# Performance work log

Hardware: AMD Instinct MI355X
Metric: run time of the kernel (lower is better)

Reference implementation:

```python
import jax, jax.numpy as jnp
import numpy as np

DIM = 1024
HEADS = 16
HEAD_DIM = DIM // HEADS
SCALE = HEAD_DIM ** -0.5


def setup_inputs() -> dict:
    key = jax.random.key(0)
    k1, k2, k3, k4 = jax.random.split(key, 4)
    x = jax.random.normal(k1, (8, 1024, DIM), dtype=jnp.float32)
    # qkv: Linear(dim, 3*dim), bias=False; proj: Linear(dim, dim) with bias
    w_qkv = jax.random.normal(k2, (DIM, 3 * DIM), dtype=jnp.float32) * (DIM ** -0.5)
    w_proj = jax.random.normal(k3, (DIM, DIM), dtype=jnp.float32) * (DIM ** -0.5)
    b_proj = jax.random.normal(k4, (DIM,), dtype=jnp.float32) * 0.02
    return {"x": x, "w_qkv": w_qkv, "w_proj": w_proj, "b_proj": b_proj}


def reference(x, w_qkv, w_proj, b_proj):
    b, n, dim = x.shape
    h, d = HEADS, HEAD_DIM
    qkv = x @ w_qkv                                  # [b, n, 3*dim]
    qkv = qkv.reshape(b, n, 3, h, d)                  # split (qkv h d)
    q = jnp.transpose(qkv[:, :, 0], (0, 2, 1, 3))     # [b, h, n, d]
    k = jnp.transpose(qkv[:, :, 1], (0, 2, 1, 3))
    v = jnp.transpose(qkv[:, :, 2], (0, 2, 1, 3))
    dots = jnp.einsum('bhid,bhjd->bhij', q, k) * SCALE
    attn = jax.nn.softmax(dots, axis=-1)              # [b, h, n, n]
    out = jnp.einsum('bhij,bhjd->bhid', attn, v)      # [b, h, n, d]
    out = jnp.transpose(out, (0, 2, 1, 3)).reshape(b, n, dim)
    return out @ w_proj + b_proj
```

## Files before the change

### kernel.cpp

```cpp
#include <hip/hip_runtime.h>
#include <hip/hip_bf16.h>
#include <stdint.h>


typedef __attribute__((ext_vector_type(8))) short  short8;
typedef __attribute__((ext_vector_type(4))) float  floatx4;

#define MFMA_BF16(a, b, c) __builtin_amdgcn_mfma_f32_16x16x32_bf16((a), (b), (c), 0, 0, 0)

__device__ __forceinline__ uint16_t f2b(float f) {
    uint32_t i; __builtin_memcpy(&i, &f, 4);
    uint32_t r = i + 0x7FFFu + ((i >> 16) & 1u);
    return (uint16_t)(r >> 16);
}

#if defined(__has_builtin)
#if __has_builtin(__builtin_amdgcn_cvt_pk_bf16_f32)
#define HAVE_PK_BF16 1
#endif
#endif

__device__ __forceinline__ uint32_t pk_bf16(float a, float b) {
#ifdef HAVE_PK_BF16
    typedef __attribute__((ext_vector_type(2))) __bf16 bf16x2;
    bf16x2 v = __builtin_amdgcn_cvt_pk_bf16_f32(a, b);
    uint32_t u; __builtin_memcpy(&u, &v, 4); return u;
#else
    return (uint32_t)f2b(a) | ((uint32_t)f2b(b) << 16);
#endif
}

__device__ __forceinline__ void async16(uint16_t* lds, const uint16_t* g) {
    __builtin_amdgcn_global_load_lds(
        (const __attribute__((address_space(1))) uint32_t*)g,
        (__attribute__((address_space(3))) uint32_t*)lds,
        16, 0, 0);
}

__global__ __launch_bounds__(256) void cvt_f32_bf16(
    const float* __restrict__ in, uint16_t* __restrict__ out, int n4)
{
    const int i = blockIdx.x * 256 + threadIdx.x;
    if (i < n4) {
        const float4 v = ((const float4*)in)[i];
        ushort4 o;
        o.x = f2b(v.x); o.y = f2b(v.y); o.z = f2b(v.z); o.w = f2b(v.w);
        ((ushort4*)out)[i] = o;
    }
}

__global__ __launch_bounds__(256) void transpose_k(
    const float* __restrict__ in, uint16_t* __restrict__ out, int R, int C)
{
    __shared__ uint16_t t[32][33];
    const int bx = blockIdx.x * 32;
    const int by = blockIdx.y * 32;
    const int tx = threadIdx.x & 31, ty = threadIdx.x >> 5;
    #pragma unroll
    for (int j = 0; j < 32; j += 8)
        t[ty + j][tx] = f2b(in[(size_t)(by + ty + j) * C + bx + tx]);
    __syncthreads();
    #pragma unroll
    for (int j = 0; j < 32; j += 8)
        out[(size_t)(bx + ty + j) * R + by + tx] = t[tx][ty + j];
}

template <int EPI>
__global__ __launch_bounds__(256, 2) void gemm_bt(
    const uint16_t* __restrict__ A, const uint16_t* __restrict__ Bt,
    uint16_t* __restrict__ C, float* __restrict__ Cf,
    const float* __restrict__ bias, int M, int N, int K)
{
    __shared__ uint16_t As[128 * 64];
    __shared__ uint16_t Bs[128 * 64];

    const int tid  = threadIdx.x;
    const int lane = tid & 63, quad = lane >> 4, l16 = lane & 15;
    const int wv   = tid >> 6;
    const int wm   = (wv >> 1) * 64, wn = (wv & 1) * 64;

    const int lid = blockIdx.y * gridDim.x + blockIdx.x;
    const int nxl = gridDim.x >> 3;
    const int xcd = lid & 7, loc = lid >> 3;
    const int bx  = xcd * nxl + (loc % nxl);
    const int by  = loc / nxl;
    const int tm  = by * 128, tn = bx * 128;

    floatx4 acc[4][4] = {};

    for (int kt = 0; kt < K; kt += 64) {
        __syncthreads();
        #pragma unroll
        for (int i = 0; i < 4; i++) {
            const int li  = i * 256 + tid;
            const int row = li >> 3;
            const int cg  = (li & 7) ^ (row & 7);
            async16(&As[li * 8], &A[(size_t)(tm + row) * K + kt + cg * 8]);
        }
        #pragma unroll
        for (int i = 0; i < 4; i++) {
            const int li  = i * 256 + tid;
            const int row = li >> 3;
            const int cg  = (li & 7) ^ (row & 7);
            async16(&Bs[li * 8], &Bt[(size_t)(tn + row) * K + kt + cg * 8]);
        }
        __syncthreads();
        #pragma unroll
        for (int kc = 0; kc < 2; kc++) {
            short8 af[4], bf[4];
            #pragma unroll
            for (int mb = 0; mb < 4; mb++) {
                const int row = wm + mb * 16 + l16;
                const int g   = kc * 4 + quad;
                af[mb] = *(const short8*)&As[row * 64 + ((g ^ (row & 7)) * 8)];
            }
            #pragma unroll
            for (int nb = 0; nb < 4; nb++) {
                const int row = wn + nb * 16 + l16;
                const int g   = kc * 4 + quad;
                bf[nb] = *(const short8*)&Bs[row * 64 + ((g ^ (row & 7)) * 8)];
            }
            #pragma unroll
            for (int mb = 0; mb < 4; mb++)
                #pragma unroll
                for (int nb = 0; nb < 4; nb++)
                    acc[mb][nb] = MFMA_BF16(af[mb], bf[nb], acc[mb][nb]);
        }
    }

    if (EPI == 0) {
        const int which = (tn + wn) >> 10;
        if (which == 2) {
            #pragma unroll
            for (int nb = 0; nb < 4; nb++) {
                const int col = tn + wn + nb * 16 + l16;
                const int hh = (col >> 6) & 15, dd = col & 63;
                #pragma unroll
                for (int mb = 0; mb < 4; mb++) {
                    const int gm = tm + wm + mb * 16 + quad * 4;
                    const int b  = gm >> 10, n = gm & 1023;
                    const size_t rgn = (size_t)(256 + b * 16 + hh) * 65536;
                    uint2 o;
                    o.x = pk_bf16(acc[mb][nb][0], acc[mb][nb][1]);
                    o.y = pk_bf16(acc[mb][nb][2], acc[mb][nb][3]);
                    *(uint2*)&C[rgn + (size_t)dd * 1024 + n] = o;
                }
            }
        } else {
            const float qs = (which == 0) ? 0.18033688011112043f : 1.0f;
            #pragma unroll
            for (int nb = 0; nb < 4; nb++) {
                const int col = tn + wn + nb * 16 + l16;
                const int hh = (col >> 6) & 15, dd = col & 63;
                #pragma unroll
                for (int mb = 0; mb < 4; mb++)
                    #pragma unroll
                    for (int r = 0; r < 4; r++) {
                        const int gm = tm + wm + mb * 16 + quad * 4 + r;
                        const int b  = gm >> 10, n = gm & 1023;
                        const size_t rgn = (size_t)(which * 128 + b * 16 + hh) * 65536;
                        C[rgn + (size_t)n * 64 + dd] = f2b(acc[mb][nb][r] * qs);
                    }
            }
        }
    } else {
        #pragma unroll
        for (int nb = 0; nb < 4; nb++) {
            const int col = tn + wn + nb * 16 + l16;
            const float bv = bias[col];
            #pragma unroll
            for (int mb = 0; mb < 4; mb++)
                #pragma unroll
                for (int r = 0; r < 4; r++) {
                    const int gm = tm + wm + mb * 16 + quad * 4 + r;
                    Cf[(size_t)gm * N + col] = acc[mb][nb][r] + bv;
                }
        }
    }
}

__global__ __launch_bounds__(256, 3) void attn_fa(
    const uint16_t* __restrict__ qkv, uint16_t* __restrict__ out)
{
    __shared__ uint16_t Ks[128 * 64];
    __shared__ uint16_t Vs[64 * 128];
    __shared__ uint16_t Ps[4][32 * 72];

    const int tid  = threadIdx.x;
    const int lane = tid & 63, quad = lane >> 4, l16 = lane & 15;
    const int wv   = tid >> 6;
    const int bh   = blockIdx.y;
    const int q0   = blockIdx.x * 128 + wv * 32;

    const size_t qbase  = (size_t)bh * 65536;
    const size_t kbase  = (size_t)(128 + bh) * 65536;
    const size_t vtbase = (size_t)(256 + bh) * 65536;

    short8 qf[2][2];
    #pragma unroll
    for (int nq = 0; nq < 2; nq++)
        #pragma unroll
        for (int ks = 0; ks < 2; ks++)
            qf[nq][ks] = *(const short8*)&qkv[qbase + (size_t)(q0 + nq * 16 + l16) * 64 + ks * 32 + quad * 8];

    floatx4 Oacc[2][4] = {};
    float lpart[2] = {0.f, 0.f};

    for (int kb = 0; kb < 8; kb++) {
        __syncthreads();
        #pragma unroll
        for (int i = 0; i < 4; i++) {
            const int li  = i * 256 + tid;
            const int row = li >> 3;
            const int cg  = (li & 7) ^ (row & 7);
            async16(&Ks[li * 8], &qkv[kbase + (size_t)(kb * 128 + row) * 64 + cg * 8]);
        }
        #pragma unroll
        for (int i = 0; i < 4; i++) {
            const int li  = i * 256 + tid;
            const int row = li >> 4;
            const int cg  = (li & 15) ^ (row & 15);
            async16(&Vs[li * 8], &qkv[vtbase + (size_t)row * 1024 + kb * 128 + cg * 8]);
        }
        __syncthreads();

        #pragma unroll
        for (int h = 0; h < 2; h++) {
            floatx4 st[4][2];
            #pragma unroll
            for (int mb = 0; mb < 4; mb++) {
                const int krow = h * 64 + mb * 16 + l16;
                const int g0 = quad, g1 = 4 + quad;
                short8 kf0 = *(const short8*)&Ks[krow * 64 + ((g0 ^ (krow & 7)) * 8)];
                short8 kf1 = *(const short8*)&Ks[krow * 64 + ((g1 ^ (krow & 7)) * 8)];
                #pragma unroll
                for (int nq = 0; nq < 2; nq++) {
                    floatx4 z = {};
                    z = MFMA_BF16(kf0, qf[nq][0], z);
                    z = MFMA_BF16(kf1, qf[nq][1], z);
                    st[mb][nq] = z;
                }
            }
            #pragma unroll
            for (int mb = 0; mb < 4; mb++)
                #pragma unroll
                for (int nq = 0; nq < 2; nq++)
                    #pragma unroll
                    for (int r = 0; r < 4; r++) {
                        const float p = exp2f(st[mb][nq][r]);
                        st[mb][nq][r] = p;
                        lpart[nq] += p;
                    }
            #pragma unroll
            for (int nq = 0; nq < 2; nq++)
                #pragma unroll
                for (int mb = 0; mb < 4; mb++) {
                    uint2 w;
                    w.x = pk_bf16(st[mb][nq][0], st[mb][nq][1]);
                    w.y = pk_bf16(st[mb][nq][2], st[mb][nq][3]);
                    *(uint2*)&Ps[wv][(nq * 16 + l16) * 72 + mb * 16 + quad * 4] = w;
                }
            short8 pf[2][2];
            #pragma unroll
            for (int qb = 0; qb < 2; qb++)
                #pragma unroll
                for (int kk = 0; kk < 2; kk++)
                    pf[qb][kk] = *(const short8*)&Ps[wv][(qb * 16 + l16) * 72 + kk * 32 + quad * 8];
            #pragma unroll
            for (int nb = 0; nb < 4; nb++)
                #pragma unroll
                for (int kk = 0; kk < 2; kk++) {
                    const int vrow = nb * 16 + l16;
                    const int g    = h * 8 + kk * 4 + quad;
                    short8 vf = *(const short8*)&Vs[vrow * 128 + ((g ^ (vrow & 15)) * 8)];
                    #pragma unroll
                    for (int qb = 0; qb < 2; qb++)
                        Oacc[qb][nb] = MFMA_BF16(pf[qb][kk], vf, Oacc[qb][nb]);
                }
        }
    }

    float linv[2];
    #pragma unroll
    for (int nq = 0; nq < 2; nq++) {
        float l = lpart[nq];
        l += __shfl_xor(l, 16);
        l += __shfl_xor(l, 32);
        linv[nq] = 1.f / l;
    }
    float inv[2][4];
    #pragma unroll
    for (int qb = 0; qb < 2; qb++)
        #pragma unroll
        for (int r = 0; r < 4; r++)
            inv[qb][r] = __shfl(linv[qb], quad * 4 + r);

    const int b = bh >> 4, hh = bh & 15;
    #pragma unroll
    for (int qb = 0; qb < 2; qb++)
        #pragma unroll
        for (int nb = 0; nb < 4; nb++)
            #pragma unroll
            for (int r = 0; r < 4; r++) {
                const int n = q0 + qb * 16 + quad * 4 + r;
                out[((size_t)(b * 1024 + n)) * 1024 + hh * 64 + nb * 16 + l16] =
                    f2b(Oacc[qb][nb][r] * inv[qb][r]);
            }
}

extern "C" void kernel_launch(void* const* d_in, const int* in_sizes, int n_in,
                              void* d_out, int out_size, void* d_ws, size_t ws_size,
                              hipStream_t stream)
{
    const float* x      = (const float*)d_in[0];
    const float* w_qkv  = (const float*)d_in[1];
    const float* w_proj = (const float*)d_in[2];
    const float* b_proj = (const float*)d_in[3];
    float* out = (float*)d_out;

    uint16_t* ws   = (uint16_t*)d_ws;
    uint16_t* xb   = ws;
    uint16_t* wTq  = xb  + 8192 * 1024;
    uint16_t* wTp  = wTq + 3072 * 1024;
    uint16_t* qkvb = wTp + 1024 * 1024;
    uint16_t* ao   = xb;

    cvt_f32_bf16<<<8192, 256, 0, stream>>>(x, xb, 8192 * 1024 / 4);
    transpose_k<<<dim3(96, 32), 256, 0, stream>>>(w_qkv, wTq, 1024, 3072);
    transpose_k<<<dim3(32, 32), 256, 0, stream>>>(w_proj, wTp, 1024, 1024);
    gemm_bt<0><<<dim3(24, 64), 256, 0, stream>>>(xb, wTq, qkvb, nullptr, nullptr, 8192, 3072, 1024);
    attn_fa<<<dim3(8, 128), 256, 0, stream>>>(qkvb, ao);
    gemm_bt<1><<<dim3(8, 64), 256, 0, stream>>>(ao, wTp, nullptr, out, b_proj, 8192, 1024, 1024);
}
```

Before: 242.9 us.

## Redistribute softmax probabilities via permlane swaps instead of an LDS round-trip

Replaces the per-wave LDS staging buffer used to convert the QK^T MFMA output layout into the A-operand layout for the PV MFMA with in-register v_permlane32/16_swap lane exchanges. This removes LDS writes and reads plus their latency, and frees shared memory, which is why the launch-bounds occupancy hint is raised from 3 to 5. It also switches exp2f to the hardware exp2 builtin when available. The risks are register pressure under the higher occupancy target, and the permlane instructions existing only on newer CDNA targets.

```diff
diff --git a/kernel.cpp b/kernel.cpp
--- a/kernel.cpp
+++ b/kernel.cpp
@@ -18,6 +18,12 @@
 #if __has_builtin(__builtin_amdgcn_cvt_pk_bf16_f32)
 #define HAVE_PK_BF16 1
 #endif
+#if __has_builtin(__builtin_amdgcn_exp2f)
+#define EXP2F __builtin_amdgcn_exp2f
+#endif
+#endif
+#ifndef EXP2F
+#define EXP2F exp2f
 #endif
 
 __device__ __forceinline__ uint32_t pk_bf16(float a, float b) {
@@ -28,6 +34,13 @@
 #else
     return (uint32_t)f2b(a) | ((uint32_t)f2b(b) << 16);
 #endif
+}
+
+__device__ __forceinline__ void p32swap(uint32_t& a, uint32_t& b) {
+    asm("v_permlane32_swap_b32 %0, %1" : "+v"(a), "+v"(b));
+}
+__device__ __forceinline__ void p16swap(uint32_t& a, uint32_t& b) {
+    asm("v_permlane16_swap_b32 %0, %1" : "+v"(a), "+v"(b));
 }
 
 __device__ __forceinline__ void async16(uint16_t* lds, const uint16_t* g) {
@@ -179,12 +192,11 @@
     }
 }
 
-__global__ __launch_bounds__(256, 3) void attn_fa(
+__global__ __launch_bounds__(256, 5) void attn_fa(
     const uint16_t* __restrict__ qkv, uint16_t* __restrict__ out)
 {
     __shared__ uint16_t Ks[128 * 64];
     __shared__ uint16_t Vs[64 * 128];
-    __shared__ uint16_t Ps[4][32 * 72];
 
     const int tid  = threadIdx.x;
     const int lane = tid & 63, quad = lane >> 4, l16 = lane & 15;
@@ -247,25 +259,24 @@
                 for (int nq = 0; nq < 2; nq++)
                     #pragma unroll
                     for (int r = 0; r < 4; r++) {
-                        const float p = exp2f(st[mb][nq][r]);
+                        const float p = EXP2F(st[mb][nq][r]);
                         st[mb][nq][r] = p;
                         lpart[nq] += p;
                     }
+            short8 pf[2][2];
             #pragma unroll
             for (int nq = 0; nq < 2; nq++)
                 #pragma unroll
-                for (int mb = 0; mb < 4; mb++) {
-                    uint2 w;
-                    w.x = pk_bf16(st[mb][nq][0], st[mb][nq][1]);
-                    w.y = pk_bf16(st[mb][nq][2], st[mb][nq][3]);
-                    *(uint2*)&Ps[wv][(nq * 16 + l16) * 72 + mb * 16 + quad * 4] = w;
-                }
-            short8 pf[2][2];
-            #pragma unroll
-            for (int qb = 0; qb < 2; qb++)
-                #pragma unroll
-                for (int kk = 0; kk < 2; kk++)
-                    pf[qb][kk] = *(const short8*)&Ps[wv][(qb * 16 + l16) * 72 + kk * 32 + quad * 8];
+                for (int kk = 0; kk < 2; kk++) {
+                    uint32_t w0 = pk_bf16(st[2 * kk][nq][0],     st[2 * kk][nq][1]);
+                    uint32_t w1 = pk_bf16(st[2 * kk][nq][2],     st[2 * kk][nq][3]);
+                    uint32_t w2 = pk_bf16(st[2 * kk + 1][nq][0], st[2 * kk + 1][nq][1]);
+                    uint32_t w3 = pk_bf16(st[2 * kk + 1][nq][2], st[2 * kk + 1][nq][3]);
+                    p32swap(w0, w2); p16swap(w0, w2);
+                    p32swap(w1, w3); p16swap(w1, w3);
+                    uint32_t w[4] = { w0, w1, w2, w3 };
+                    __builtin_memcpy(&pf[nq][kk], w, 16);
+                }
             #pragma unroll
             for (int nb = 0; nb < 4; nb++)
                 #pragma unroll
```

Measured after the change: 304.1 us. +25.2%, slower.
